# Performance work log

Hardware: AMD Instinct MI355X
Metric: run time of the kernel (lower is better)

Reference implementation:

```python
import jax, jax.numpy as jnp
import numpy as np

EPS = 1e-5

def _bn(z, g, b):
    # train-mode BatchNorm2d: batch stats over (B,H,W), biased variance
    mean = z.mean(axis=(0, 2, 3), keepdims=True)
    var = z.var(axis=(0, 2, 3), keepdims=True)
    return g[None, :, None, None] * (z - mean) * jax.lax.rsqrt(var + EPS) + b[None, :, None, None]

def _conv1x1(x, w):
    # x: [B,C,H,W], w: [O,C] -> [B,O,H,W]
    return jnp.einsum('bchw,oc->bohw', x, w)

def _proj(x, w1, g1, b1, w2, g2, b2):
    z = _bn(_conv1x1(x, w1), g1, b1)
    return _bn(_conv1x1(z, w2), g2, b2)

def setup_inputs() -> dict:
    key = jax.random.key(0)
    ks = jax.random.split(key, 24)
    B, Cx, Cy, M, H, W = 4, 512, 256, 64, 64, 64
    f32 = jnp.float32
    def wmat(k, o, c):
        return jax.random.normal(k, (o, c), f32) * (c ** -0.5)
    def gamma(k, c):
        return 1.0 + 0.1 * jax.random.normal(k, (c,), f32)
    def beta(k, c):
        return 0.1 * jax.random.normal(k, (c,), f32)
    inp = {
        'x': jax.random.normal(ks[0], (B, Cx, H, W), f32),
        'y': jax.random.normal(ks[1], (B, Cy, H, W), f32),
        # f_self
        'ws1': wmat(ks[2], M, Cx), 'gs1': gamma(ks[3], M), 'bs1': beta(ks[4], M),
        'ws2': wmat(ks[5], M, M),  'gs2': gamma(ks[6], M), 'bs2': beta(ks[7], M),
        # f_x
        'wx1': wmat(ks[8], M, Cx), 'gx1': gamma(ks[9], M), 'bx1': beta(ks[10], M),
        'wx2': wmat(ks[11], M, M), 'gx2': gamma(ks[12], M), 'bx2': beta(ks[13], M),
        # f_y
        'wy1': wmat(ks[14], M, Cy), 'gy1': gamma(ks[15], M), 'by1': beta(ks[16], M),
        'wy2': wmat(ks[17], M, M),  'gy2': gamma(ks[18], M), 'by2': beta(ks[19], M),
        # f_up
        'wu': wmat(ks[20], Cx, M), 'gu': gamma(ks[21], Cx), 'bu': beta(ks[22], Cx),
    }
    return inp

def reference(x, y, ws1, gs1, bs1, ws2, gs2, bs2,
              wx1, gx1, bx1, wx2, gx2, bx2,
              wy1, gy1, by1, wy2, gy2, by2,
              wu, gu, bu):
    B, C, H, W = x.shape
    M = ws1.shape[0]
    N = H * W
    fself = _proj(x, ws1, gs1, bs1, ws2, gs2, bs2).reshape(B, M, N).transpose(0, 2, 1)  # [B,N,M]
    fx = _proj(x, wx1, gx1, bx1, wx2, gx2, bx2).reshape(B, M, N).transpose(0, 2, 1)      # [B,N,M]
    fy = _proj(y, wy1, gy1, by1, wy2, gy2, by2).reshape(B, M, N)                          # [B,M,N]
    sim = jnp.matmul(fx, fy)                  # [B,N,N]  (scale=False)
    attn = jax.nn.softmax(sim, axis=-1)
    fout = jnp.matmul(attn, fself)            # [B,N,M]
    fout = fout.transpose(0, 2, 1).reshape(B, M, H, W)
    out = _bn(_conv1x1(fout, wu), gu, bu)
    return x + out
```

## Files before the change

### kernel.cpp

```cpp
#include <hip/hip_runtime.h>
#include <hip/hip_fp16.h>
#include <cstdint>

constexpr int N_ = 4096;
constexpr float CNT = 16384.f;

typedef __attribute__((ext_vector_type(8))) _Float16 half8;
typedef __attribute__((ext_vector_type(4))) float f32x4;
union fragh { half8 h8; int i4[4]; };

__device__ inline int pkh(float a, float b) {
  union { __half2 h; int i; } u;
  u.h = __float22half2_rn(float2{a, b});
  return u.i;
}
__device__ inline void pk_hl(float a, float b, int& h, int& l) {
  __half ah = __float2half_rn(a), bh = __float2half_rn(b);
  union { __half2 v; int i; } u;
  u.v = __halves2half2(ah, bh);
  h = u.i;
  float ar = a - __half2float(ah), br = b - __half2float(bh);
  union { __half2 v; int i; } w2;
  w2.v = __float22half2_rn(float2{ar, br});
  l = w2.i;
}
__device__ inline float2 uph(int v) {
  union { __half2 h; int i; } u;
  u.i = v;
  return float2{__half2float(__low2half(u.h)), __half2float(__high2half(u.h))};
}


__global__ __launch_bounds__(256) void packA_k(const float* __restrict__ x,
                                               const float* __restrict__ y,
                                               int* __restrict__ Afx,
                                               int* __restrict__ Afy) {
  const int job = blockIdx.y;
  if (job == 1 && blockIdx.x >= 2048) return;
  const int idx = blockIdx.x * 256 + threadIdx.x;
  const float* src = job ? y : x;
  int* dst = job ? Afy : Afx;
  const int KT = job ? 8 : 16;
  const int loOff = job ? 2097152 : 4194304;
  const int n = idx & 4095, q = (idx >> 12) & 3;
  const int kt = job ? ((idx >> 14) & 7) : ((idx >> 14) & 15);
  const int b = job ? (idx >> 17) : (idx >> 18);
  const float* sp = src + ((size_t)(b * (KT * 32) + kt * 32 + q * 8)) * N_ + n;
  float a[8];
#pragma unroll
  for (int j = 0; j < 8; ++j) a[j] = sp[(size_t)j * N_];
  int4 hi, lo;
  pk_hl(a[0], a[1], hi.x, lo.x);
  pk_hl(a[2], a[3], hi.y, lo.y);
  pk_hl(a[4], a[5], hi.z, lo.z);
  pk_hl(a[6], a[7], hi.w, lo.w);
  const int base = (((b * KT + kt) * 256 + (n >> 4)) * 64 + q * 16 + (n & 15)) * 4;
  *(int4*)&dst[base] = hi;
  *(int4*)&dst[loOff + base] = lo;
}

__global__ __launch_bounds__(256) void prep1_k(const float* __restrict__ ws1,
                                               const float* __restrict__ wx1,
                                               const float* __restrict__ wy1,
                                               int* __restrict__ wt1f) {
  const int idx = blockIdx.x * 256 + threadIdx.x;
  const float* W;
  int KT, K, hiBase, loOff, e;
  if (idx < 16384) { W = ws1; KT = 16; K = 512; hiBase = 0; loOff = 16384; e = idx; }
  else if (idx < 32768) { W = wx1; KT = 16; K = 512; hiBase = 32768; loOff = 16384; e = idx - 16384; }
  else { W = wy1; KT = 8; K = 256; hiBase = 65536; loOff = 8192; e = idx - 32768; }
  const int jj = e & 3, lane = (e >> 2) & 63;
  int kt, ot;
  if (KT == 16) { kt = (e >> 8) & 15; ot = e >> 12; } else { kt = (e >> 8) & 7; ot = e >> 11; }
  const int o = ot * 16 + (lane & 15);
  const int k = kt * 32 + (lane >> 4) * 8 + 2 * jj;
  int h, l;
  pk_hl(W[o * K + k], W[o * K + k + 1], h, l);
  wt1f[hiBase + e] = h;
  wt1f[hiBase + loOff + e] = l;
}

__global__ __launch_bounds__(256) void prep2_k(
    const float* __restrict__ ws2, const float* __restrict__ wx2,
    const float* __restrict__ wy2,
    const float* __restrict__ gs1, const float* __restrict__ bs1,
    const float* __restrict__ gx1, const float* __restrict__ bx1,
    const float* __restrict__ gy1, const float* __restrict__ by1,
    const float* __restrict__ stats, int* __restrict__ wt2f,
    float* __restrict__ biasf) {
  const int branch = blockIdx.x;
  const int t = threadIdx.x;
  const float* W = branch == 0 ? ws2 : (branch == 1 ? wx2 : wy2);
  const float* g1 = branch == 0 ? gs1 : (branch == 1 ? gx1 : gy1);
  const float* b1 = branch == 0 ? bs1 : (branch == 1 ? bx1 : by1);
  const float* stin = stats + branch * 128;
  int* outW = wt2f + branch * 4096;

  auto scale = [&](int k) {
    float mean = stin[k] * (1.f / CNT);
    float var = stin[64 + k] * (1.f / CNT) - mean * mean;
    return g1[k] * rsqrtf(var + 1e-5f);
  };
#pragma unroll
  for (int i = 0; i < 8; ++i) {
    int e = i * 256 + t;
    int jj = e & 3, lane = (e >> 2) & 63, kt = (e >> 8) & 1, ot = e >> 9;
    int o = ot * 16 + (lane & 15);
    int k = kt * 32 + (lane >> 4) * 8 + 2 * jj;
    float w0 = W[o * 64 + k] * scale(k);
    float w1 = W[o * 64 + k + 1] * scale(k + 1);
    int h, l;
    pk_hl(w0, w1, h, l);
    outW[e] = h;
    outW[2048 + e] = l;
  }
  if (t < 64) {
    float s = 0.f;
    for (int k = 0; k < 64; ++k) {
      float mean = stin[k] * (1.f / CNT);
      float var = stin[64 + k] * (1.f / CNT) - mean * mean;
      float sc = g1[k] * rsqrtf(var + 1e-5f);
      float sh = b1[k] - mean * sc;
      s += W[t * 64 + k] * sh;
    }
    biasf[branch * 64 + t] = s;
  }
}

__global__ __launch_bounds__(256) void prepu_k(const float* __restrict__ wu,
                                               float* __restrict__ wut) {
  int e = blockIdx.x * 256 + threadIdx.x;
  int k = e >> 9, o = e & 511;
  wut[e] = wu[o * 64 + k];
}

__global__ __launch_bounds__(256) void conv1_k(
    const int* __restrict__ Afx, const int* __restrict__ Afy,
    const int* __restrict__ wt1f, int* __restrict__ z1f,
    float* __restrict__ stats) {
  const int t = threadIdx.x;
  const int lane = t & 63;
  const int wv = t >> 6;
  const int la = lane & 15;
  const int quad = lane >> 4;
  const int b = blockIdx.x >> 4;
  const int ns = blockIdx.x & 15;
  const int branch = blockIdx.y;
  const int KT = branch == 2 ? 8 : 16;
  const int* Af = branch == 2 ? Afy : Afx;
  const int aLo = branch == 2 ? 2097152 : 4194304;
  const int* Wf = wt1f + (branch == 0 ? 0 : (branch == 1 ? 32768 : 65536));
  const int wLo = branch == 2 ? 8192 : 16384;
  float* st = stats + branch * 128;
  int* zb = z1f + branch * 1048576;

  f32x4 acc[4][4];
#pragma unroll
  for (int i = 0; i < 4; ++i)
#pragma unroll
    for (int j = 0; j < 4; ++j) acc[i][j] = f32x4{0.f, 0.f, 0.f, 0.f};

  const int ntg0 = ns * 16 + wv * 4;
#pragma unroll 1
  for (int kt = 0; kt < KT; ++kt) {
    fragh wh[4], wl[4], ah[4], al[4];
#pragma unroll
    for (int ot = 0; ot < 4; ++ot) {
      const int base = ((ot * KT + kt) * 64 + lane) * 4;
      *(int4*)wh[ot].i4 = *(const int4*)&Wf[base];
      *(int4*)wl[ot].i4 = *(const int4*)&Wf[wLo + base];
    }
#pragma unroll
    for (int nt = 0; nt < 4; ++nt) {
      const int base = (((b * KT + kt) * 256 + ntg0 + nt) * 64 + lane) * 4;
      *(int4*)ah[nt].i4 = *(const int4*)&Af[base];
      *(int4*)al[nt].i4 = *(const int4*)&Af[aLo + base];
    }
#pragma unroll
    for (int ot = 0; ot < 4; ++ot)
#pragma unroll
      for (int nt = 0; nt < 4; ++nt) {
        acc[ot][nt] = __builtin_amdgcn_mfma_f32_16x16x32_f16(wh[ot].h8, ah[nt].h8, acc[ot][nt], 0, 0, 0);
        acc[ot][nt] = __builtin_amdgcn_mfma_f32_16x16x32_f16(wh[ot].h8, al[nt].h8, acc[ot][nt], 0, 0, 0);
        acc[ot][nt] = __builtin_amdgcn_mfma_f32_16x16x32_f16(wl[ot].h8, ah[nt].h8, acc[ot][nt], 0, 0, 0);
      }
  }
#pragma unroll
  for (int ot = 0; ot < 4; ++ot) {
    const int ktz = ot >> 1;
    const int qz = (ot & 1) * 2 + (quad >> 1);
    const int jz = (quad & 1) * 2;
#pragma unroll
    for (int nt = 0; nt < 4; ++nt) {
      const int addr = (((b * 2 + ktz) * 256 + ntg0 + nt) * 64 + qz * 16 + la) * 4 + jz;
      int h0, l0, h1, l1;
      pk_hl(acc[ot][nt][0], acc[ot][nt][1], h0, l0);
      pk_hl(acc[ot][nt][2], acc[ot][nt][3], h1, l1);
      *(int2*)&zb[addr] = int2{h0, h1};
      *(int2*)&zb[524288 + addr] = int2{l0, l1};
    }
  }
#pragma unroll
  for (int ot = 0; ot < 4; ++ot)
#pragma unroll
    for (int r = 0; r < 4; ++r) {
      float s = acc[ot][0][r] + acc[ot][1][r] + acc[ot][2][r] + acc[ot][3][r];
      float q = acc[ot][0][r] * acc[ot][0][r] + acc[ot][1][r] * acc[ot][1][r] +
                acc[ot][2][r] * acc[ot][2][r] + acc[ot][3][r] * acc[ot][3][r];
#pragma unroll
      for (int d = 1; d < 16; d <<= 1) { s += __shfl_xor(s, d); q += __shfl_xor(q, d); }
      if (la == 0) {
        atomicAdd(&st[ot * 16 + quad * 4 + r], s);
        atomicAdd(&st[64 + ot * 16 + quad * 4 + r], q);
      }
    }
}

__global__ __launch_bounds__(256) void conv2_k(
    const int* __restrict__ z1f, const int* __restrict__ wt2f,
    const float* __restrict__ biasf, int* __restrict__ z2f,
    float* __restrict__ stats) {
  const int t = threadIdx.x;
  const int lane = t & 63;
  const int wv = t >> 6;
  const int la = lane & 15;
  const int quad = lane >> 4;
  const int b = blockIdx.x >> 4;
  const int ns = blockIdx.x & 15;
  const int branch = blockIdx.y;
  const int* Af = z1f + branch * 1048576;
  const int* Wf = wt2f + branch * 4096;
  const float* bias = biasf + branch * 64;
  float* st = stats + (3 + branch) * 128;
  int* zb = z2f + branch * 1048576;

  f32x4 acc[4][4];
#pragma unroll
  for (int ot = 0; ot < 4; ++ot)
#pragma unroll
    for (int nt = 0; nt < 4; ++nt) {
#pragma unroll
      for (int r = 0; r < 4; ++r) acc[ot][nt][r] = bias[ot * 16 + quad * 4 + r];
    }

  const int ntg0 = ns * 16 + wv * 4;
#pragma unroll 1
  for (int kt = 0; kt < 2; ++kt) {
    fragh wh[4], wl[4], ah[4], al[4];
#pragma unroll
    for (int ot = 0; ot < 4; ++ot) {
      const int base = ((ot * 2 + kt) * 64 + lane) * 4;
      *(int4*)wh[ot].i4 = *(const int4*)&Wf[base];
      *(int4*)wl[ot].i4 = *(const int4*)&Wf[2048 + base];
    }
#pragma unroll
    for (int nt = 0; nt < 4; ++nt) {
      const int base = (((b * 2 + kt) * 256 + ntg0 + nt) * 64 + lane) * 4;
      *(int4*)ah[nt].i4 = *(const int4*)&Af[base];
      *(int4*)al[nt].i4 = *(const int4*)&Af[524288 + base];
    }
#pragma unroll
    for (int ot = 0; ot < 4; ++ot)
#pragma unroll
      for (int nt = 0; nt < 4; ++nt) {
        acc[ot][nt] = __builtin_amdgcn_mfma_f32_16x16x32_f16(wh[ot].h8, ah[nt].h8, acc[ot][nt], 0, 0, 0);
        acc[ot][nt] = __builtin_amdgcn_mfma_f32_16x16x32_f16(wh[ot].h8, al[nt].h8, acc[ot][nt], 0, 0, 0);
        acc[ot][nt] = __builtin_amdgcn_mfma_f32_16x16x32_f16(wl[ot].h8, ah[nt].h8, acc[ot][nt], 0, 0, 0);
      }
  }
#pragma unroll
  for (int ot = 0; ot < 4; ++ot) {
    const int ktz = ot >> 1;
    const int qz = (ot & 1) * 2 + (quad >> 1);
    const int jz = (quad & 1) * 2;
#pragma unroll
    for (int nt = 0; nt < 4; ++nt) {
      const int addr = (((b * 2 + ktz) * 256 + ntg0 + nt) * 64 + qz * 16 + la) * 4 + jz;
      int h0, l0, h1, l1;
      pk_hl(acc[ot][nt][0], acc[ot][nt][1], h0, l0);
      pk_hl(acc[ot][nt][2], acc[ot][nt][3], h1, l1);
      *(int2*)&zb[addr] = int2{h0, h1};
      *(int2*)&zb[524288 + addr] = int2{l0, l1};
    }
  }
#pragma unroll
  for (int ot = 0; ot < 4; ++ot)
#pragma unroll
    for (int r = 0; r < 4; ++r) {
      float s = acc[ot][0][r] + acc[ot][1][r] + acc[ot][2][r] + acc[ot][3][r];
      float q = acc[ot][0][r] * acc[ot][0][r] + acc[ot][1][r] * acc[ot][1][r] +
                acc[ot][2][r] * acc[ot][2][r] + acc[ot][3][r] * acc[ot][3][r];
#pragma unroll
      for (int d = 1; d < 16; d <<= 1) { s += __shfl_xor(s, d); q += __shfl_xor(q, d); }
      if (la == 0) {
        atomicAdd(&st[ot * 16 + quad * 4 + r], s);
        atomicAdd(&st[64 + ot * 16 + quad * 4 + r], q);
      }
    }
}

__global__ __launch_bounds__(256) void pack_k(
    const int* __restrict__ z2f,
    const float* __restrict__ gs2, const float* __restrict__ bs2,
    const float* __restrict__ gx2, const float* __restrict__ bx2,
    const float* __restrict__ gy2, const float* __restrict__ by2,
    int* __restrict__ Qf, int* __restrict__ Kf, int* __restrict__ Vf,
    const float* __restrict__ stats) {
  const int job = blockIdx.z;
  const int idx = blockIdx.x * 256 + threadIdx.x;
  const float* g2 = job == 0 ? gx2 : (job == 1 ? gy2 : gs2);
  const float* b2 = job == 0 ? bx2 : (job == 1 ? by2 : bs2);
  const float* st = stats + (job == 0 ? 4 : (job == 1 ? 5 : 3)) * 128;

  auto snorm = [&](int c, float& s, float& h) {
    float mean = st[c] * (1.f / CNT);
    float var = st[64 + c] * (1.f / CNT) - mean * mean;
    float r = rsqrtf(var + 1e-5f);
    s = g2[c] * r;
    h = b2[c] - mean * s;
  };
  if (job < 2) {
    const int* zf = z2f + (job == 0 ? 1048576 : 2097152);
    int* outp = job == 0 ? Qf : Kf;
    int h = zf[idx], l = zf[524288 + idx];
    int jj = idx & 3, lane = (idx >> 2) & 63, q = lane >> 4;
    int kt = (idx >> 16) & 1;
    int c0 = 2 * (kt * 16 + q * 4 + jj);
    float s0, h0, s1, h1;
    snorm(c0, s0, h0);
    snorm(c0 + 1, s1, h1);
    float2 vh = uph(h), vl = uph(l);
    outp[idx] = pkh((vh.x + vl.x) * s0 + h0, (vh.y + vl.y) * s1 + h1);
  } else {
    int w_ = idx & 3, lane = (idx >> 2) & 63, la_v = lane & 15, q_v = lane >> 4;
    int mt = (idx >> 8) & 3, kb = (idx >> 10) & 127, b = idx >> 17;
    int ch = mt * 16 + la_v;
    int k = kb * 16 + q_v * 4 + w_;
    int n0 = 2 * k;
    int kp = ch >> 1, kt = kp >> 4, qz = (kp >> 2) & 3, jz = kp & 3, half = ch & 1;
    int a0 = (((b * 2 + kt) * 256 + (n0 >> 4)) * 64 + qz * 16 + (n0 & 15)) * 4 + jz;
    float2 h0v = uph(z2f[a0]), l0v = uph(z2f[524288 + a0]);
    float2 h1v = uph(z2f[a0 + 4]), l1v = uph(z2f[524288 + a0 + 4]);
    float v0 = half ? (h0v.y + l0v.y) : (h0v.x + l0v.x);
    float v1 = half ? (h1v.y + l1v.y) : (h1v.x + l1v.x);
    float s0, h0;
    snorm(ch, s0, h0);
    Vf[idx] = pkh(v0 * s0 + h0, v1 * s0 + h0);
  }
}

__global__ __launch_bounds__(256, 4) void attn_k(const int* __restrict__ Qf,
                                                 const int* __restrict__ Kf,
                                                 const int* __restrict__ Vf,
                                                 float* __restrict__ fout) {
  const int tid = threadIdx.x;
  const int lane = tid & 63;
  const int wid = tid >> 6;
  const int la = lane & 15;
  const int quad = lane >> 4;
  const int b = blockIdx.x & 3;
  const int qbase = (blockIdx.x >> 2) * 16;
  const int* Qb = Qf + (size_t)b * 131072;
  const int* Kb4 = Kf + (size_t)b * 131072;
  const int* Vb4 = Vf + (size_t)b * 131072;

  __shared__ union USm {
    int P16[4][16 * 20];
    struct { float O[4][16][69]; float M[4][16]; float L[4][16]; } e;
  } smu;
  int* myP = smu.P16[wid];

  fragh aq[2];
#pragma unroll
  for (int c = 0; c < 2; ++c)
    *(int4*)aq[c].i4 =
        *(const int4*)&Qb[((c * 256 + (qbase >> 4)) * 64 + quad * 16 + la) * 4];

  f32x4 o[4];
  float mrun = -3.0e38f, lrun = 0.f;
#pragma unroll
  for (int mt = 0; mt < 4; ++mt) o[mt] = f32x4{0.f, 0.f, 0.f, 0.f};

  const int jbeg = wid * (N_ / 4);
  const int jend = jbeg + N_ / 4;

  int4 ka[2][2], kb2[2][2];
#pragma unroll
  for (int nt = 0; nt < 2; ++nt)
#pragma unroll
    for (int g = 0; g < 2; ++g)
      ka[nt][g] = *(const int4*)&Kb4[((g * 256 + (jbeg >> 4) + nt) * 64 + lane) * 4];

  auto body = [&](int j0, int4 (&kc)[2][2], int4 (&kn)[2][2]) {
    f32x4 s[2];
#pragma unroll
    for (int nt = 0; nt < 2; ++nt) {
      fragh k0, k1;
      k0.i4[0] = kc[nt][0].x; k0.i4[1] = kc[nt][0].y;
      k0.i4[2] = kc[nt][0].z; k0.i4[3] = kc[nt][0].w;
      k1.i4[0] = kc[nt][1].x; k1.i4[1] = kc[nt][1].y;
      k1.i4[2] = kc[nt][1].z; k1.i4[3] = kc[nt][1].w;
      f32x4 z = f32x4{0.f, 0.f, 0.f, 0.f};
      z = __builtin_amdgcn_mfma_f32_16x16x32_f16(k0.h8, aq[0].h8, z, 0, 0, 0);
      s[nt] = __builtin_amdgcn_mfma_f32_16x16x32_f16(k1.h8, aq[1].h8, z, 0, 0, 0);
    }
    int4 vv[4];
#pragma unroll
    for (int mt = 0; mt < 4; ++mt)
      vv[mt] = *(const int4*)&Vb4[(((j0 >> 5) * 4 + mt) * 64 + lane) * 4];
    const int nj = (j0 + 32 < jend) ? (j0 + 32) : jbeg;
#pragma unroll
    for (int nt = 0; nt < 2; ++nt)
#pragma unroll
      for (int g = 0; g < 2; ++g)
        kn[nt][g] = *(const int4*)&Kb4[((g * 256 + (nj >> 4) + nt) * 64 + lane) * 4];
    float t0 = fmaxf(fmaxf(s[0][0], s[0][1]), fmaxf(s[0][2], s[0][3]));
    float t1 = fmaxf(fmaxf(s[1][0], s[1][1]), fmaxf(s[1][2], s[1][3]));
    float t = fmaxf(t0, t1);
    t = fmaxf(t, __shfl_xor(t, 16));
    t = fmaxf(t, __shfl_xor(t, 32));
    float mnew = fmaxf(mrun, t);
    float alpha = __expf(mrun - mnew);
    float p[2][4];
    float ps = 0.f;
#pragma unroll
    for (int nt = 0; nt < 2; ++nt)
#pragma unroll
      for (int r = 0; r < 4; ++r) {
        p[nt][r] = __expf(s[nt][r] - mnew);
        ps += p[nt][r];
      }
    ps += __shfl_xor(ps, 16);
    ps += __shfl_xor(ps, 32);
    lrun = lrun * alpha + ps;
    mrun = mnew;
#pragma unroll
    for (int nt = 0; nt < 2; ++nt) {
      myP[(nt * 8 + quad * 2 + 0) * 20 + la] = pkh(p[nt][0], p[nt][1]);
      myP[(nt * 8 + quad * 2 + 1) * 20 + la] = pkh(p[nt][2], p[nt][3]);
    }
    __asm__ __volatile__("s_waitcnt lgkmcnt(0)" ::: "memory");
    fragh pb;
#pragma unroll
    for (int j = 0; j < 4; ++j) pb.i4[j] = myP[(quad * 4 + j) * 20 + la];
#pragma unroll
    for (int mt = 0; mt < 4; ++mt) {
      o[mt][0] *= alpha; o[mt][1] *= alpha;
      o[mt][2] *= alpha; o[mt][3] *= alpha;
    }
#pragma unroll
    for (int mt = 0; mt < 4; ++mt) {
      fragh vb;
      vb.i4[0] = vv[mt].x; vb.i4[1] = vv[mt].y;
      vb.i4[2] = vv[mt].z; vb.i4[3] = vv[mt].w;
      o[mt] = __builtin_amdgcn_mfma_f32_16x16x32_f16(vb.h8, pb.h8, o[mt], 0, 0, 0);
    }
  };

#pragma unroll 1
  for (int j0 = jbeg; j0 < jend; j0 += 64) {
    body(j0, ka, kb2);
    body(j0 + 32, kb2, ka);
  }

  __syncthreads();
  if (quad == 0) {
    smu.e.M[wid][la] = mrun;
    smu.e.L[wid][la] = lrun;
  }
#pragma unroll
  for (int mt = 0; mt < 4; ++mt)
#pragma unroll
    for (int r = 0; r < 4; ++r) smu.e.O[wid][la][mt * 16 + quad * 4 + r] = o[mt][r];
  __syncthreads();

#pragma unroll
  for (int t = 0; t < 4; ++t) {
    int oidx = t * 256 + tid;
    int m = oidx >> 4;
    int q = oidx & 15;
    float m0 = fmaxf(fmaxf(smu.e.M[0][q], smu.e.M[1][q]),
                     fmaxf(smu.e.M[2][q], smu.e.M[3][q]));
    float num = 0.f, den = 0.f;
#pragma unroll
    for (int w = 0; w < 4; ++w) {
      float wgt = __expf(smu.e.M[w][q] - m0);
      num += wgt * smu.e.O[w][q][m];
      den += wgt * smu.e.L[w][q];
    }
    fout[((size_t)b * 64 + m) * N_ + qbase + q] = num / den;
  }
}

__global__ __launch_bounds__(256) void convup_k(const float* __restrict__ fout,
                                                const float* __restrict__ wut,
                                                float* __restrict__ u,
                                                float* __restrict__ stats) {
  const int t = threadIdx.x;
  const int b = blockIdx.x >> 4;
  const int n0 = (blockIdx.x & 15) * 256;
  const int o0 = blockIdx.y * 64;

  __shared__ float sA[16][260];
  __shared__ float sW[16][68];

  const int ng4 = (t & 31) * 4;
  const int og8 = (t >> 5) * 8;
  float acc[8][8];
#pragma unroll
  for (int i = 0; i < 8; ++i)
#pragma unroll
    for (int j = 0; j < 8; ++j) acc[i][j] = 0.f;

  const float* Ap = fout + ((size_t)b * 64 + (t >> 6)) * N_ + n0 + (t & 63) * 4;
  const float* Wp = wut + (size_t)(t >> 4) * 512 + o0 + (t & 15) * 4;
  const int arow = t >> 6, acol = (t & 63) * 4;
  const int wrow = t >> 4, wcol = (t & 15) * 4;

  float4 pa[4];
  float4 pw;
#pragma unroll
  for (int i = 0; i < 4; ++i) pa[i] = *(const float4*)(Ap + (size_t)(4 * i) * N_);
  pw = *(const float4*)Wp;
  Ap += (size_t)16 * N_;
  Wp += 16 * 512;
#pragma unroll
  for (int i = 0; i < 4; ++i) *(float4*)&sA[arow + 4 * i][acol] = pa[i];
  *(float4*)&sW[wrow][wcol] = pw;
  __syncthreads();

#pragma unroll 1
  for (int k0 = 0; k0 < 64; k0 += 16) {
    const bool more = (k0 + 16) < 64;
    if (more) {
#pragma unroll
      for (int i = 0; i < 4; ++i) pa[i] = *(const float4*)(Ap + (size_t)(4 * i) * N_);
      pw = *(const float4*)Wp;
      Ap += (size_t)16 * N_;
      Wp += 16 * 512;
    }
#pragma unroll
    for (int k = 0; k < 16; ++k) {
      float4 a0 = *(const float4*)&sA[k][ng4];
      float4 a1 = *(const float4*)&sA[k][128 + ng4];
      float4 w0 = *(const float4*)&sW[k][og8];
      float4 w1 = *(const float4*)&sW[k][og8 + 4];
      float av[8] = {a0.x, a0.y, a0.z, a0.w, a1.x, a1.y, a1.z, a1.w};
      float wv[8] = {w0.x, w0.y, w0.z, w0.w, w1.x, w1.y, w1.z, w1.w};
#pragma unroll
      for (int i = 0; i < 8; ++i)
#pragma unroll
        for (int j = 0; j < 8; ++j) acc[i][j] = fmaf(wv[i], av[j], acc[i][j]);
    }
    __syncthreads();
    if (more) {
#pragma unroll
      for (int i = 0; i < 4; ++i) *(float4*)&sA[arow + 4 * i][acol] = pa[i];
      *(float4*)&sW[wrow][wcol] = pw;
    }
    __syncthreads();
  }

  float* Cb = u + ((size_t)b * 512 + o0 + og8) * N_ + n0;
#pragma unroll
  for (int i = 0; i < 8; ++i) {
    float4 v0 = {acc[i][0], acc[i][1], acc[i][2], acc[i][3]};
    float4 v1 = {acc[i][4], acc[i][5], acc[i][6], acc[i][7]};
    *(float4*)&Cb[(size_t)i * N_ + ng4] = v0;
    *(float4*)&Cb[(size_t)i * N_ + 128 + ng4] = v1;
  }
#pragma unroll
  for (int i = 0; i < 8; ++i) {
    float s = 0.f, q = 0.f;
#pragma unroll
    for (int j = 0; j < 8; ++j) { s += acc[i][j]; q += acc[i][j] * acc[i][j]; }
#pragma unroll
    for (int d = 1; d < 32; d <<= 1) { s += __shfl_xor(s, d); q += __shfl_xor(q, d); }
    if ((t & 31) == 0) {
      atomicAdd(&stats[768 + o0 + og8 + i], s);
      atomicAdd(&stats[1280 + o0 + og8 + i], q);
    }
  }
}

__global__ __launch_bounds__(256) void final_k(const float* __restrict__ x,
                                               const float* __restrict__ u,
                                               const float* __restrict__ gu,
                                               const float* __restrict__ bu,
                                               const float* __restrict__ stats,
                                               float* __restrict__ out) {
  size_t idx = (size_t)blockIdx.x * 256 + threadIdx.x;
  int c = (int)((idx >> 12) & 511);
  float mean = stats[768 + c] * (1.f / CNT);
  float var = stats[1280 + c] * (1.f / CNT) - mean * mean;
  float r = rsqrtf(var + 1e-5f);
  float s = gu[c] * r;
  float sh = bu[c] - mean * s;
  out[idx] = x[idx] + u[idx] * s + sh;
}

extern "C" void kernel_launch(void* const* d_in, const int* in_sizes, int n_in,
                              void* d_out, int out_size, void* d_ws, size_t ws_size,
                              hipStream_t stream) {
  const float* x = (const float*)d_in[0];
  const float* y = (const float*)d_in[1];
  const float* ws1 = (const float*)d_in[2];
  const float* gs1 = (const float*)d_in[3];
  const float* bs1 = (const float*)d_in[4];
  const float* ws2 = (const float*)d_in[5];
  const float* gs2 = (const float*)d_in[6];
  const float* bs2 = (const float*)d_in[7];
  const float* wx1 = (const float*)d_in[8];
  const float* gx1 = (const float*)d_in[9];
  const float* bx1 = (const float*)d_in[10];
  const float* wx2 = (const float*)d_in[11];
  const float* gx2 = (const float*)d_in[12];
  const float* bx2 = (const float*)d_in[13];
  const float* wy1 = (const float*)d_in[14];
  const float* gy1 = (const float*)d_in[15];
  const float* by1 = (const float*)d_in[16];
  const float* wy2 = (const float*)d_in[17];
  const float* gy2 = (const float*)d_in[18];
  const float* by2 = (const float*)d_in[19];
  const float* wu = (const float*)d_in[20];
  const float* gu = (const float*)d_in[21];
  const float* bu = (const float*)d_in[22];
  float* out = (float*)d_out;

  float* w = (float*)d_ws;
  const size_t M1 = 1048576;
  int* z1f = (int*)w;
  int* z2f = (int*)(w + 3 * M1);
  float* fout = w + 6 * M1;
  float* u = w + 7 * M1;
  int* Afx = (int*)u;
  int* Afy = (int*)(w + 3 * M1);
  int* Qf = (int*)(w + 15 * M1);
  int* Kf = Qf + 524288;
  int* Vf = Kf + 524288;
  float* stats = (float*)(Vf + 524288);
  int* wt1f = (int*)(stats + 1792);
  int* wt2f = wt1f + 81920;
  float* biasf = (float*)(wt2f + 12288);
  float* wut = biasf + 192;

  hipMemsetAsync(stats, 0, 1792 * sizeof(float), stream);

  prep1_k<<<dim3(160), dim3(256), 0, stream>>>(ws1, wx1, wy1, wt1f);
  packA_k<<<dim3(4096, 2), dim3(256), 0, stream>>>(x, y, Afx, Afy);
  conv1_k<<<dim3(64, 3), dim3(256), 0, stream>>>(Afx, Afy, wt1f, z1f, stats);
  prep2_k<<<dim3(3), dim3(256), 0, stream>>>(ws2, wx2, wy2, gs1, bs1, gx1, bx1,
                                             gy1, by1, stats, wt2f, biasf);
  conv2_k<<<dim3(64, 3), dim3(256), 0, stream>>>(z1f, wt2f, biasf, z2f, stats);
  prepu_k<<<dim3(128), dim3(256), 0, stream>>>(wu, wut);
  pack_k<<<dim3(2048, 1, 3), dim3(256), 0, stream>>>(z2f, gs2, bs2, gx2, bx2, gy2,
                                                     by2, Qf, Kf, Vf, stats);
  attn_k<<<dim3(1024), dim3(256), 0, stream>>>(Qf, Kf, Vf, fout);
  convup_k<<<dim3(64, 8), dim3(256), 0, stream>>>(fout, wut, u, stats);
  final_k<<<dim3(32768), dim3(256), 0, stream>>>(x, u, gu, bu, stats, out);
}
```

Before: 368.5 us.

## Port up-projection conv to split-fp16 MFMA and shrink conv1/conv2 tiles

The up-projection 1x1 conv changes from an fp32 FMA shared-memory GEMM to split-fp16 (hi/lo) MFMA. Its weights and the attention output are now packed into MFMA fragment layout: attn_k writes packed fp16 hi/lo directly instead of fp32, and prepu_k packs wu. conv1 and conv2 now compute one N-tile per wave instead of four, which quadruples the grid, and conv1 double-buffers its fragment loads. The smaller tiles add parallelism and cut register use, but weight fragments are reused less, and the strided scalar stores in convup may coalesce poorly.

```diff
diff --git a/kernel.cpp b/kernel.cpp
--- a/kernel.cpp
+++ b/kernel.cpp
@@ -128,10 +128,15 @@
 }
 
 __global__ __launch_bounds__(256) void prepu_k(const float* __restrict__ wu,
-                                               float* __restrict__ wut) {
-  int e = blockIdx.x * 256 + threadIdx.x;
-  int k = e >> 9, o = e & 511;
-  wut[e] = wu[o * 64 + k];
+                                               int* __restrict__ wuf) {
+  const int e = blockIdx.x * 256 + threadIdx.x;
+  const int jj = e & 3, lane = (e >> 2) & 63, kt = (e >> 8) & 1, otg = e >> 9;
+  const int o = otg * 16 + (lane & 15);
+  const int m = kt * 32 + (lane >> 4) * 8 + 2 * jj;
+  int h, l;
+  pk_hl(wu[o * 64 + m], wu[o * 64 + m + 1], h, l);
+  wuf[e] = h;
+  wuf[16384 + e] = l;
 }
 
 __global__ __launch_bounds__(256) void conv1_k(
@@ -143,8 +148,8 @@
   const int wv = t >> 6;
   const int la = lane & 15;
   const int quad = lane >> 4;
-  const int b = blockIdx.x >> 4;
-  const int ns = blockIdx.x & 15;
+  const int b = blockIdx.x >> 6;
+  const int ns = blockIdx.x & 63;
   const int branch = blockIdx.y;
   const int KT = branch == 2 ? 8 : 16;
   const int* Af = branch == 2 ? Afy : Afx;
@@ -153,60 +158,61 @@
   const int wLo = branch == 2 ? 8192 : 16384;
   float* st = stats + branch * 128;
   int* zb = z1f + branch * 1048576;
-
-  f32x4 acc[4][4];
-#pragma unroll
-  for (int i = 0; i < 4; ++i)
-#pragma unroll
-    for (int j = 0; j < 4; ++j) acc[i][j] = f32x4{0.f, 0.f, 0.f, 0.f};
-
-  const int ntg0 = ns * 16 + wv * 4;
-#pragma unroll 1
-  for (int kt = 0; kt < KT; ++kt) {
-    fragh wh[4], wl[4], ah[4], al[4];
+  const int ntg0 = ns * 4 + wv;
+
+  f32x4 acc[4];
+#pragma unroll
+  for (int ot = 0; ot < 4; ++ot) acc[ot] = f32x4{0.f, 0.f, 0.f, 0.f};
+
+  auto loadF = [&](int kt, fragh (&wh)[4], fragh (&wl)[4], fragh& ah, fragh& al) {
 #pragma unroll
     for (int ot = 0; ot < 4; ++ot) {
       const int base = ((ot * KT + kt) * 64 + lane) * 4;
       *(int4*)wh[ot].i4 = *(const int4*)&Wf[base];
       *(int4*)wl[ot].i4 = *(const int4*)&Wf[wLo + base];
     }
-#pragma unroll
-    for (int nt = 0; nt < 4; ++nt) {
-      const int base = (((b * KT + kt) * 256 + ntg0 + nt) * 64 + lane) * 4;
-      *(int4*)ah[nt].i4 = *(const int4*)&Af[base];
-      *(int4*)al[nt].i4 = *(const int4*)&Af[aLo + base];
-    }
-#pragma unroll
-    for (int ot = 0; ot < 4; ++ot)
-#pragma unroll
-      for (int nt = 0; nt < 4; ++nt) {
-        acc[ot][nt] = __builtin_amdgcn_mfma_f32_16x16x32_f16(wh[ot].h8, ah[nt].h8, acc[ot][nt], 0, 0, 0);
-        acc[ot][nt] = __builtin_amdgcn_mfma_f32_16x16x32_f16(wh[ot].h8, al[nt].h8, acc[ot][nt], 0, 0, 0);
-        acc[ot][nt] = __builtin_amdgcn_mfma_f32_16x16x32_f16(wl[ot].h8, ah[nt].h8, acc[ot][nt], 0, 0, 0);
-      }
-  }
+    const int abase = (((b * KT + kt) * 256 + ntg0) * 64 + lane) * 4;
+    *(int4*)ah.i4 = *(const int4*)&Af[abase];
+    *(int4*)al.i4 = *(const int4*)&Af[aLo + abase];
+  };
+  auto mm = [&](fragh (&wh)[4], fragh (&wl)[4], fragh& ah, fragh& al) {
+#pragma unroll
+    for (int ot = 0; ot < 4; ++ot) {
+      acc[ot] = __builtin_amdgcn_mfma_f32_16x16x32_f16(wh[ot].h8, ah.h8, acc[ot], 0, 0, 0);
+      acc[ot] = __builtin_amdgcn_mfma_f32_16x16x32_f16(wh[ot].h8, al.h8, acc[ot], 0, 0, 0);
+      acc[ot] = __builtin_amdgcn_mfma_f32_16x16x32_f16(wl[ot].h8, ah.h8, acc[ot], 0, 0, 0);
+    }
+  };
+
+  fragh whA[4], wlA[4], ahA, alA;
+  fragh whB[4], wlB[4], ahB, alB;
+  loadF(0, whA, wlA, ahA, alA);
+#pragma unroll 1
+  for (int kt = 0; kt < KT; kt += 2) {
+    loadF(kt + 1, whB, wlB, ahB, alB);
+    mm(whA, wlA, ahA, alA);
+    if (kt + 2 < KT) loadF(kt + 2, whA, wlA, ahA, alA);
+    mm(whB, wlB, ahB, alB);
+  }
+
 #pragma unroll
   for (int ot = 0; ot < 4; ++ot) {
     const int ktz = ot >> 1;
     const int qz = (ot & 1) * 2 + (quad >> 1);
     const int jz = (quad & 1) * 2;
-#pragma unroll
-    for (int nt = 0; nt < 4; ++nt) {
-      const int addr = (((b * 2 + ktz) * 256 + ntg0 + nt) * 64 + qz * 16 + la) * 4 + jz;
-      int h0, l0, h1, l1;
-      pk_hl(acc[ot][nt][0], acc[ot][nt][1], h0, l0);
-      pk_hl(acc[ot][nt][2], acc[ot][nt][3], h1, l1);
-      *(int2*)&zb[addr] = int2{h0, h1};
-      *(int2*)&zb[524288 + addr] = int2{l0, l1};
-    }
+    const int addr = (((b * 2 + ktz) * 256 + ntg0) * 64 + qz * 16 + la) * 4 + jz;
+    int h0, l0, h1, l1;
+    pk_hl(acc[ot][0], acc[ot][1], h0, l0);
+    pk_hl(acc[ot][2], acc[ot][3], h1, l1);
+    *(int2*)&zb[addr] = int2{h0, h1};
+    *(int2*)&zb[524288 + addr] = int2{l0, l1};
   }
 #pragma unroll
   for (int ot = 0; ot < 4; ++ot)
 #pragma unroll
     for (int r = 0; r < 4; ++r) {
-      float s = acc[ot][0][r] + acc[ot][1][r] + acc[ot][2][r] + acc[ot][3][r];
-      float q = acc[ot][0][r] * acc[ot][0][r] + acc[ot][1][r] * acc[ot][1][r] +
-                acc[ot][2][r] * acc[ot][2][r] + acc[ot][3][r] * acc[ot][3][r];
+      float s = acc[ot][r];
+      float q = s * s;
 #pragma unroll
       for (int d = 1; d < 16; d <<= 1) { s += __shfl_xor(s, d); q += __shfl_xor(q, d); }
       if (la == 0) {
@@ -225,71 +231,68 @@
   const int wv = t >> 6;
   const int la = lane & 15;
   const int quad = lane >> 4;
-  const int b = blockIdx.x >> 4;
-  const int ns = blockIdx.x & 15;
+  const int b = blockIdx.x >> 6;
+  const int ns = blockIdx.x & 63;
   const int branch = blockIdx.y;
   const int* Af = z1f + branch * 1048576;
   const int* Wf = wt2f + branch * 4096;
   const float* bias = biasf + branch * 64;
   float* st = stats + (3 + branch) * 128;
   int* zb = z2f + branch * 1048576;
-
-  f32x4 acc[4][4];
-#pragma unroll
-  for (int ot = 0; ot < 4; ++ot)
-#pragma unroll
-    for (int nt = 0; nt < 4; ++nt) {
-#pragma unroll
-      for (int r = 0; r < 4; ++r) acc[ot][nt][r] = bias[ot * 16 + quad * 4 + r];
-    }
-
-  const int ntg0 = ns * 16 + wv * 4;
-#pragma unroll 1
-  for (int kt = 0; kt < 2; ++kt) {
-    fragh wh[4], wl[4], ah[4], al[4];
+  const int ntg0 = ns * 4 + wv;
+
+  f32x4 acc[4];
+#pragma unroll
+  for (int ot = 0; ot < 4; ++ot) {
+#pragma unroll
+    for (int r = 0; r < 4; ++r) acc[ot][r] = bias[ot * 16 + quad * 4 + r];
+  }
+
+  auto loadF = [&](int kt, fragh (&wh)[4], fragh (&wl)[4], fragh& ah, fragh& al) {
 #pragma unroll
     for (int ot = 0; ot < 4; ++ot) {
       const int base = ((ot * 2 + kt) * 64 + lane) * 4;
       *(int4*)wh[ot].i4 = *(const int4*)&Wf[base];
       *(int4*)wl[ot].i4 = *(const int4*)&Wf[2048 + base];
     }
-#pragma unroll
-    for (int nt = 0; nt < 4; ++nt) {
-      const int base = (((b * 2 + kt) * 256 + ntg0 + nt) * 64 + lane) * 4;
-      *(int4*)ah[nt].i4 = *(const int4*)&Af[base];
-      *(int4*)al[nt].i4 = *(const int4*)&Af[524288 + base];
-    }
-#pragma unroll
-    for (int ot = 0; ot < 4; ++ot)
-#pragma unroll
-      for (int nt = 0; nt < 4; ++nt) {
-        acc[ot][nt] = __builtin_amdgcn_mfma_f32_16x16x32_f16(wh[ot].h8, ah[nt].h8, acc[ot][nt], 0, 0, 0);
-        acc[ot][nt] = __builtin_amdgcn_mfma_f32_16x16x32_f16(wh[ot].h8, al[nt].h8, acc[ot][nt], 0, 0, 0);
-        acc[ot][nt] = __builtin_amdgcn_mfma_f32_16x16x32_f16(wl[ot].h8, ah[nt].h8, acc[ot][nt], 0, 0, 0);
-      }
-  }
+    const int abase = (((b * 2 + kt) * 256 + ntg0) * 64 + lane) * 4;
+    *(int4*)ah.i4 = *(const int4*)&Af[abase];
+    *(int4*)al.i4 = *(const int4*)&Af[524288 + abase];
+  };
+  auto mm = [&](fragh (&wh)[4], fragh (&wl)[4], fragh& ah, fragh& al) {
+#pragma unroll
+    for (int ot = 0; ot < 4; ++ot) {
+      acc[ot] = __builtin_amdgcn_mfma_f32_16x16x32_f16(wh[ot].h8, ah.h8, acc[ot], 0, 0, 0);
+      acc[ot] = __builtin_amdgcn_mfma_f32_16x16x32_f16(wh[ot].h8, al.h8, acc[ot], 0, 0, 0);
+      acc[ot] = __builtin_amdgcn_mfma_f32_16x16x32_f16(wl[ot].h8, ah.h8, acc[ot], 0, 0, 0);
+    }
+  };
+
+  fragh whA[4], wlA[4], ahA, alA;
+  fragh whB[4], wlB[4], ahB, alB;
+  loadF(0, whA, wlA, ahA, alA);
+  loadF(1, whB, wlB, ahB, alB);
+  mm(whA, wlA, ahA, alA);
+  mm(whB, wlB, ahB, alB);
+
 #pragma unroll
   for (int ot = 0; ot < 4; ++ot) {
     const int ktz = ot >> 1;
     const int qz = (ot & 1) * 2 + (quad >> 1);
     const int jz = (quad & 1) * 2;
-#pragma unroll
-    for (int nt = 0; nt < 4; ++nt) {
-      const int addr = (((b * 2 + ktz) * 256 + ntg0 + nt) * 64 + qz * 16 + la) * 4 + jz;
-      int h0, l0, h1, l1;
-      pk_hl(acc[ot][nt][0], acc[ot][nt][1], h0, l0);
-      pk_hl(acc[ot][nt][2], acc[ot][nt][3], h1, l1);
-      *(int2*)&zb[addr] = int2{h0, h1};
-      *(int2*)&zb[524288 + addr] = int2{l0, l1};
-    }
+    const int addr = (((b * 2 + ktz) * 256 + ntg0) * 64 + qz * 16 + la) * 4 + jz;
+    int h0, l0, h1, l1;
+    pk_hl(acc[ot][0], acc[ot][1], h0, l0);
+    pk_hl(acc[ot][2], acc[ot][3], h1, l1);
+    *(int2*)&zb[addr] = int2{h0, h1};
+    *(int2*)&zb[524288 + addr] = int2{l0, l1};
   }
 #pragma unroll
   for (int ot = 0; ot < 4; ++ot)
 #pragma unroll
     for (int r = 0; r < 4; ++r) {
-      float s = acc[ot][0][r] + acc[ot][1][r] + acc[ot][2][r] + acc[ot][3][r];
-      float q = acc[ot][0][r] * acc[ot][0][r] + acc[ot][1][r] * acc[ot][1][r] +
-                acc[ot][2][r] * acc[ot][2][r] + acc[ot][3][r] * acc[ot][3][r];
+      float s = acc[ot][r];
+      float q = s * s;
 #pragma unroll
       for (int d = 1; d < 16; d <<= 1) { s += __shfl_xor(s, d); q += __shfl_xor(q, d); }
       if (la == 0) {
@@ -352,7 +355,7 @@
 __global__ __launch_bounds__(256, 4) void attn_k(const int* __restrict__ Qf,
                                                  const int* __restrict__ Kf,
                                                  const int* __restrict__ Vf,
-                                                 float* __restrict__ fout) {
+                                                 int* __restrict__ foutf) {
   const int tid = threadIdx.x;
   const int lane = tid & 63;
   const int wid = tid >> 6;
@@ -475,112 +478,107 @@
   __syncthreads();
 
 #pragma unroll
-  for (int t = 0; t < 4; ++t) {
-    int oidx = t * 256 + tid;
-    int m = oidx >> 4;
-    int q = oidx & 15;
+  for (int t = 0; t < 2; ++t) {
+    int pidx = t * 256 + tid;
+    int p = pidx >> 4;
+    int q = pidx & 15;
     float m0 = fmaxf(fmaxf(smu.e.M[0][q], smu.e.M[1][q]),
                      fmaxf(smu.e.M[2][q], smu.e.M[3][q]));
-    float num = 0.f, den = 0.f;
+    float num0 = 0.f, num1 = 0.f, den = 0.f;
 #pragma unroll
     for (int w = 0; w < 4; ++w) {
       float wgt = __expf(smu.e.M[w][q] - m0);
-      num += wgt * smu.e.O[w][q][m];
+      num0 += wgt * smu.e.O[w][q][2 * p];
+      num1 += wgt * smu.e.O[w][q][2 * p + 1];
       den += wgt * smu.e.L[w][q];
     }
-    fout[((size_t)b * 64 + m) * N_ + qbase + q] = num / den;
-  }
-}
-
-__global__ __launch_bounds__(256) void convup_k(const float* __restrict__ fout,
-                                                const float* __restrict__ wut,
+    float inv = 1.f / den;
+    int h, l;
+    pk_hl(num0 * inv, num1 * inv, h, l);
+    int kt = p >> 4, qz = (p >> 2) & 3, jj = p & 3;
+    int addr = (((b * 2 + kt) * 256 + (qbase >> 4)) * 64 + qz * 16 + q) * 4 + jj;
+    foutf[addr] = h;
+    foutf[524288 + addr] = l;
+  }
+}
+
+__global__ __launch_bounds__(256) void convup_k(const int* __restrict__ foutf,
+                                                const int* __restrict__ wuf,
                                                 float* __restrict__ u,
                                                 float* __restrict__ stats) {
   const int t = threadIdx.x;
-  const int b = blockIdx.x >> 4;
-  const int n0 = (blockIdx.x & 15) * 256;
-  const int o0 = blockIdx.y * 64;
-
-  __shared__ float sA[16][260];
-  __shared__ float sW[16][68];
-
-  const int ng4 = (t & 31) * 4;
-  const int og8 = (t >> 5) * 8;
-  float acc[8][8];
-#pragma unroll
-  for (int i = 0; i < 8; ++i)
-#pragma unroll
-    for (int j = 0; j < 8; ++j) acc[i][j] = 0.f;
-
-  const float* Ap = fout + ((size_t)b * 64 + (t >> 6)) * N_ + n0 + (t & 63) * 4;
-  const float* Wp = wut + (size_t)(t >> 4) * 512 + o0 + (t & 15) * 4;
-  const int arow = t >> 6, acol = (t & 63) * 4;
-  const int wrow = t >> 4, wcol = (t & 15) * 4;
-
-  float4 pa[4];
-  float4 pw;
-#pragma unroll
-  for (int i = 0; i < 4; ++i) pa[i] = *(const float4*)(Ap + (size_t)(4 * i) * N_);
-  pw = *(const float4*)Wp;
-  Ap += (size_t)16 * N_;
-  Wp += 16 * 512;
-#pragma unroll
-  for (int i = 0; i < 4; ++i) *(float4*)&sA[arow + 4 * i][acol] = pa[i];
-  *(float4*)&sW[wrow][wcol] = pw;
-  __syncthreads();
-
-#pragma unroll 1
-  for (int k0 = 0; k0 < 64; k0 += 16) {
-    const bool more = (k0 + 16) < 64;
-    if (more) {
-#pragma unroll
-      for (int i = 0; i < 4; ++i) pa[i] = *(const float4*)(Ap + (size_t)(4 * i) * N_);
-      pw = *(const float4*)Wp;
-      Ap += (size_t)16 * N_;
-      Wp += 16 * 512;
-    }
-#pragma unroll
-    for (int k = 0; k < 16; ++k) {
-      float4 a0 = *(const float4*)&sA[k][ng4];
-      float4 a1 = *(const float4*)&sA[k][128 + ng4];
-      float4 w0 = *(const float4*)&sW[k][og8];
-      float4 w1 = *(const float4*)&sW[k][og8 + 4];
-      float av[8] = {a0.x, a0.y, a0.z, a0.w, a1.x, a1.y, a1.z, a1.w};
-      float wv[8] = {w0.x, w0.y, w0.z, w0.w, w1.x, w1.y, w1.z, w1.w};
-#pragma unroll
-      for (int i = 0; i < 8; ++i)
-#pragma unroll
-        for (int j = 0; j < 8; ++j) acc[i][j] = fmaf(wv[i], av[j], acc[i][j]);
-    }
-    __syncthreads();
-    if (more) {
-#pragma unroll
-      for (int i = 0; i < 4; ++i) *(float4*)&sA[arow + 4 * i][acol] = pa[i];
-      *(float4*)&sW[wrow][wcol] = pw;
-    }
-    __syncthreads();
-  }
-
-  float* Cb = u + ((size_t)b * 512 + o0 + og8) * N_ + n0;
-#pragma unroll
-  for (int i = 0; i < 8; ++i) {
-    float4 v0 = {acc[i][0], acc[i][1], acc[i][2], acc[i][3]};
-    float4 v1 = {acc[i][4], acc[i][5], acc[i][6], acc[i][7]};
-    *(float4*)&Cb[(size_t)i * N_ + ng4] = v0;
-    *(float4*)&Cb[(size_t)i * N_ + 128 + ng4] = v1;
-  }
-#pragma unroll
-  for (int i = 0; i < 8; ++i) {
-    float s = 0.f, q = 0.f;
-#pragma unroll
-    for (int j = 0; j < 8; ++j) { s += acc[i][j]; q += acc[i][j] * acc[i][j]; }
-#pragma unroll
-    for (int d = 1; d < 32; d <<= 1) { s += __shfl_xor(s, d); q += __shfl_xor(q, d); }
-    if ((t & 31) == 0) {
-      atomicAdd(&stats[768 + o0 + og8 + i], s);
-      atomicAdd(&stats[1280 + o0 + og8 + i], q);
-    }
-  }
+  const int lane = t & 63;
+  const int wv = t >> 6;
+  const int la = lane & 15;
+  const int quad = lane >> 4;
+  const int b = blockIdx.x >> 5;
+  const int ns = blockIdx.x & 31;
+  const int o0g = blockIdx.y * 4;
+  const int ntg0 = ns * 8 + wv * 2;
+
+  f32x4 acc[4][2];
+#pragma unroll
+  for (int ot = 0; ot < 4; ++ot)
+#pragma unroll
+    for (int nt = 0; nt < 2; ++nt) acc[ot][nt] = f32x4{0.f, 0.f, 0.f, 0.f};
+
+  auto loadF = [&](int kt, fragh (&wh)[4], fragh (&wl)[4], fragh (&ah)[2],
+                   fragh (&al)[2]) {
+#pragma unroll
+    for (int ot = 0; ot < 4; ++ot) {
+      const int base = (((o0g + ot) * 2 + kt) * 64 + lane) * 4;
+      *(int4*)wh[ot].i4 = *(const int4*)&wuf[base];
+      *(int4*)wl[ot].i4 = *(const int4*)&wuf[16384 + base];
+    }
+#pragma unroll
+    for (int nt = 0; nt < 2; ++nt) {
+      const int abase = (((b * 2 + kt) * 256 + ntg0 + nt) * 64 + lane) * 4;
+      *(int4*)ah[nt].i4 = *(const int4*)&foutf[abase];
+      *(int4*)al[nt].i4 = *(const int4*)&foutf[524288 + abase];
+    }
+  };
+  auto mm = [&](fragh (&wh)[4], fragh (&wl)[4], fragh (&ah)[2], fragh (&al)[2]) {
+#pragma unroll
+    for (int ot = 0; ot < 4; ++ot)
+#pragma unroll
+      for (int nt = 0; nt < 2; ++nt) {
+        acc[ot][nt] = __builtin_amdgcn_mfma_f32_16x16x32_f16(wh[ot].h8, ah[nt].h8, acc[ot][nt], 0, 0, 0);
+        acc[ot][nt] = __builtin_amdgcn_mfma_f32_16x16x32_f16(wh[ot].h8, al[nt].h8, acc[ot][nt], 0, 0, 0);
+        acc[ot][nt] = __builtin_amdgcn_mfma_f32_16x16x32_f16(wl[ot].h8, ah[nt].h8, acc[ot][nt], 0, 0, 0);
+      }
+  };
+
+  fragh whA[4], wlA[4], ahA[2], alA[2];
+  fragh whB[4], wlB[4], ahB[2], alB[2];
+  loadF(0, whA, wlA, ahA, alA);
+  loadF(1, whB, wlB, ahB, alB);
+  mm(whA, wlA, ahA, alA);
+  mm(whB, wlB, ahB, alB);
+
+#pragma unroll
+  for (int ot = 0; ot < 4; ++ot)
+#pragma unroll
+    for (int nt = 0; nt < 2; ++nt) {
+#pragma unroll
+      for (int r = 0; r < 4; ++r) {
+        const int o = (o0g + ot) * 16 + quad * 4 + r;
+        u[((size_t)b * 512 + o) * N_ + (ntg0 + nt) * 16 + la] = acc[ot][nt][r];
+      }
+    }
+#pragma unroll
+  for (int ot = 0; ot < 4; ++ot)
+#pragma unroll
+    for (int r = 0; r < 4; ++r) {
+      float s = acc[ot][0][r] + acc[ot][1][r];
+      float q = acc[ot][0][r] * acc[ot][0][r] + acc[ot][1][r] * acc[ot][1][r];
+#pragma unroll
+      for (int d = 1; d < 16; d <<= 1) { s += __shfl_xor(s, d); q += __shfl_xor(q, d); }
+      if (la == 0) {
+        const int o = (o0g + ot) * 16 + quad * 4 + r;
+        atomicAdd(&stats[768 + o], s);
+        atomicAdd(&stats[1280 + o], q);
+      }
+    }
 }
 
 __global__ __launch_bounds__(256) void final_k(const float* __restrict__ x,
@@ -631,7 +629,7 @@
   const size_t M1 = 1048576;
   int* z1f = (int*)w;
   int* z2f = (int*)(w + 3 * M1);
-  float* fout = w + 6 * M1;
+  int* foutf = (int*)(w + 6 * M1);
   float* u = w + 7 * M1;
   int* Afx = (int*)u;
   int* Afy = (int*)(w + 3 * M1);
@@ -642,20 +640,20 @@
   int* wt1f = (int*)(stats + 1792);
   int* wt2f = wt1f + 81920;
   float* biasf = (float*)(wt2f + 12288);
-  float* wut = biasf + 192;
+  int* wuf = (int*)(biasf + 192);
 
   hipMemsetAsync(stats, 0, 1792 * sizeof(float), stream);
 
   prep1_k<<<dim3(160), dim3(256), 0, stream>>>(ws1, wx1, wy1, wt1f);
   packA_k<<<dim3(4096, 2), dim3(256), 0, stream>>>(x, y, Afx, Afy);
-  conv1_k<<<dim3(64, 3), dim3(256), 0, stream>>>(Afx, Afy, wt1f, z1f, stats);
+  conv1_k<<<dim3(256, 3), dim3(256), 0, stream>>>(Afx, Afy, wt1f, z1f, stats);
   prep2_k<<<dim3(3), dim3(256), 0, stream>>>(ws2, wx2, wy2, gs1, bs1, gx1, bx1,
                                              gy1, by1, stats, wt2f, biasf);
-  conv2_k<<<dim3(64, 3), dim3(256), 0, stream>>>(z1f, wt2f, biasf, z2f, stats);
-  prepu_k<<<dim3(128), dim3(256), 0, stream>>>(wu, wut);
+  conv2_k<<<dim3(256, 3), dim3(256), 0, stream>>>(z1f, wt2f, biasf, z2f, stats);
+  prepu_k<<<dim3(64), dim3(256), 0, stream>>>(wu, wuf);
   pack_k<<<dim3(2048, 1, 3), dim3(256), 0, stream>>>(z2f, gs2, bs2, gx2, bx2, gy2,
                                                      by2, Qf, Kf, Vf, stats);
-  attn_k<<<dim3(1024), dim3(256), 0, stream>>>(Qf, Kf, Vf, fout);
-  convup_k<<<dim3(64, 8), dim3(256), 0, stream>>>(fout, wut, u, stats);
+  attn_k<<<dim3(1024), dim3(256), 0, stream>>>(Qf, Kf, Vf, foutf);
+  convup_k<<<dim3(128, 8), dim3(256), 0, stream>>>(foutf, wuf, u, stats);
   final_k<<<dim3(32768), dim3(256), 0, stream>>>(x, u, gu, bu, stats, out);
 }
```

After: 681.9 us. 85.1% more time.
